# Kernel tuning notes

Measured on AMD Instinct MI355X. Metric: run time of the kernel, lower is better.

The kernel has to match this reference:

```python
import jax, jax.numpy as jnp
import numpy as np

B, L, IN_DIM, H, LAYERS = 16, 2048, 64, 512, 4
KERNELS = (5, 11, 23)
EPS_BN, EPS_LN = 1e-5, 1e-5


def setup_inputs() -> dict:
    key = jax.random.key(0)
    ks = jax.random.split(key, 16)
    def n(k, shape, s=0.02):
        return jax.random.normal(k, shape, jnp.float32) * s
    inp = {"x": jax.random.normal(ks[0], (B, L, IN_DIM), jnp.float32)}
    inp["Wp"] = n(ks[1], (H, IN_DIM), 0.1)
    inp["bp"] = jnp.zeros((H,), jnp.float32)
    inp["ln_g"] = jnp.ones((LAYERS, H), jnp.float32)
    inp["ln_b"] = jnp.zeros((LAYERS, H), jnp.float32)
    for i, k in enumerate(KERNELS):
        inp[f"conv_w{i}"] = n(ks[2 + i], (LAYERS, H, k), 0.1)  # depthwise kernels
        inp[f"conv_b{i}"] = jnp.zeros((LAYERS, H), jnp.float32)
    inp["bn_g"] = jnp.ones((LAYERS, 3, H), jnp.float32)
    inp["bn_b"] = jnp.zeros((LAYERS, 3, H), jnp.float32)
    inp["gate_W"] = n(ks[5], (LAYERS, 3, 3 * H), 0.02)
    inp["gate_b"] = jnp.zeros((LAYERS, 3), jnp.float32)
    inp["Wih"] = n(ks[6], (LAYERS, 3 * H, H), 0.04)  # GRU input weights (r,z,n)
    inp["Whh"] = n(ks[7], (LAYERS, 3 * H, H), 0.04)  # GRU hidden weights
    inp["bih"] = jnp.zeros((LAYERS, 3 * H), jnp.float32)
    inp["bhh"] = jnp.zeros((LAYERS, 3 * H), jnp.float32)
    return inp


def _layernorm(h, g, b):
    mu = h.mean(-1, keepdims=True)
    var = ((h - mu) ** 2).mean(-1, keepdims=True)
    return (h - mu) / jnp.sqrt(var + EPS_LN) * g + b


def _dwconv(h_bhl, w, b):
    # h_bhl: [B,H,L]; w: [H,k] depthwise; 'same' padding for odd k (pad=k//2)
    k = w.shape[-1]
    out = jax.lax.conv_general_dilated(
        h_bhl, w[:, None, :], (1,), [(k // 2, k // 2)],
        dimension_numbers=("NCH", "OIH", "NCH"), feature_group_count=h_bhl.shape[1])
    return out + b[None, :, None]


def _longconv_mix(h, conv_ws, conv_bs, bn_g, bn_b, gate_W, gate_b):
    # h: [B,L,H]
    ht = jnp.swapaxes(h, 1, 2)  # [B,H,L]
    bn_scale = 1.0 / jnp.sqrt(1.0 + EPS_BN)  # eval BN: running mean 0, var 1
    outs = []
    for i in range(len(conv_ws)):
        o = _dwconv(ht, conv_ws[i], conv_bs[i])
        o = o * (bn_g[i] * bn_scale)[None, :, None] + bn_b[i][None, :, None]
        outs.append(jax.nn.gelu(o, approximate=False))
    cat_t = jnp.swapaxes(jnp.concatenate(outs, axis=1), 1, 2)  # [B,L,3H]
    logits = cat_t @ gate_W.T + gate_b                          # [B,L,3]
    wgt = jax.nn.softmax(logits, axis=-1)
    stack = jnp.stack(outs, axis=1)                             # [B,3,H,L]
    out = jnp.einsum("bkhl,blk->bhl", stack, wgt)
    return jnp.swapaxes(out, 1, 2)  # [B,L,H]


def _gru(h, Wih, Whh, bih, bhh):
    # torch nn.GRU math, gate order r,z,n; h: [B,L,H]
    Bb, Ll, Hh = h.shape
    xg = jnp.swapaxes(h @ Wih.T + bih, 0, 1)  # [L,B,3H]
    def step(hp, x_t):
        hg = hp @ Whh.T + bhh
        xr, xz, xn = jnp.split(x_t, 3, axis=-1)
        hr, hz, hn = jnp.split(hg, 3, axis=-1)
        r = jax.nn.sigmoid(xr + hr)
        z = jax.nn.sigmoid(xz + hz)
        n = jnp.tanh(xn + r * hn)
        hnew = (1.0 - z) * n + z * hp
        return hnew, hnew
    _, ys = jax.lax.scan(step, jnp.zeros((Bb, Hh), h.dtype), xg)
    return jnp.swapaxes(ys, 0, 1)  # [B,L,H]


def reference(x, Wp, bp, ln_g, ln_b, conv_w0, conv_b0, conv_w1, conv_b1,
              conv_w2, conv_b2, bn_g, bn_b, gate_W, gate_b, Wih, Whh, bih, bhh):
    h = x @ Wp.T + bp  # input_proj: [B,L,H]
    for l in range(LAYERS):
        h = _layernorm(h, ln_g[l], ln_b[l])
        h = _longconv_mix(h,
                          (conv_w0[l], conv_w1[l], conv_w2[l]),
                          (conv_b0[l], conv_b1[l], conv_b2[l]),
                          bn_g[l], bn_b[l], gate_W[l], gate_b[l])
        out = _gru(h, Wih[l], Whh[l], bih[l], bhh[l])
        h = h + out  # residual (dropout=0 in eval)
    return h
```

## Files before the change

### kernel.cpp

```cpp
#include <hip/hip_runtime.h>
#include <hip/hip_bf16.h>


#define B_   16
#define L_   2048
#define IN_  64
#define H_   512
#define H3_  1536
#define NL_  4

typedef unsigned short u16;
typedef unsigned long long u64;
typedef short bf16x8 __attribute__((ext_vector_type(8)));
typedef float f32x4 __attribute__((ext_vector_type(4)));

__device__ __forceinline__ u16 f2bf(float f) {
  unsigned u = __float_as_uint(f);
  u = u + 0x7fffu + ((u >> 16) & 1u);
  return (u16)(u >> 16);
}
__device__ __forceinline__ float bf2f(u16 v) {
  return __uint_as_float(((unsigned)v) << 16);
}
__device__ __forceinline__ float gelu_exact(float x) {
  return 0.5f * x * (1.f + erff(x * 0.70710678118654752440f));
}
__device__ __forceinline__ float fast_sig(float x) {
  float e = __expf(-x);
  return __builtin_amdgcn_rcpf(1.f + e);
}
__device__ __forceinline__ float fast_tanh(float x) {
  x = fminf(fmaxf(x, -15.f), 15.f);
  float e = __expf(2.f * x);
  return (e - 1.f) * __builtin_amdgcn_rcpf(e + 1.f);
}
__device__ __forceinline__ float dotw(uint4 wp, float4 ha, float4 hc) {
  float acc;
  acc  = __uint_as_float(wp.x << 16)          * ha.x;
  acc += __uint_as_float(wp.x & 0xffff0000u)  * ha.y;
  acc += __uint_as_float(wp.y << 16)          * ha.z;
  acc += __uint_as_float(wp.y & 0xffff0000u)  * ha.w;
  acc += __uint_as_float(wp.z << 16)          * hc.x;
  acc += __uint_as_float(wp.z & 0xffff0000u)  * hc.y;
  acc += __uint_as_float(wp.w << 16)          * hc.z;
  acc += __uint_as_float(wp.w & 0xffff0000u)  * hc.w;
  return acc;
}

__global__ void k_init(u64* hst, int n) {
  int i = blockIdx.x * blockDim.x + threadIdx.x;
  if (i < n) hst[i] = 0ull;
}

__global__ void k_cvt(const float* __restrict__ in, u16* __restrict__ out, int n) {
  int i = blockIdx.x * blockDim.x + threadIdx.x;
  int stride = gridDim.x * blockDim.x;
  for (; i < n; i += stride) out[i] = f2bf(in[i]);
}

__global__ __launch_bounds__(512)
void k_proj(const float* __restrict__ x, const float* __restrict__ Wp,
            const float* __restrict__ bp, float* __restrict__ hb) {
  __shared__ float4 xs[128];
  const int tid = threadIdx.x;
  const size_t m0 = (size_t)blockIdx.x * 8;
  if (tid < 128) xs[tid] = ((const float4*)(x + m0 * IN_))[tid];
  __syncthreads();
  float4 wv[16];
  const float4* wp4 = (const float4*)(Wp + (size_t)tid * IN_);
#pragma unroll
  for (int i = 0; i < 16; ++i) wv[i] = wp4[i];
  float acc[8] = {0.f,0.f,0.f,0.f,0.f,0.f,0.f,0.f};
#pragma unroll
  for (int k = 0; k < 16; ++k) {
    float4 w4 = wv[k];
#pragma unroll
    for (int rr = 0; rr < 8; ++rr) {
      float4 xv = xs[rr * 16 + k];
      acc[rr] += w4.x * xv.x + w4.y * xv.y + w4.z * xv.z + w4.w * xv.w;
    }
  }
  float bpv = bp[tid];
#pragma unroll
  for (int rr = 0; rr < 8; ++rr) hb[(m0 + rr) * H_ + tid] = acc[rr] + bpv;
}

__global__ __launch_bounds__(256)
void k_ln(const float* __restrict__ hin, const float* __restrict__ g,
          const float* __restrict__ bta, float* __restrict__ lnout) {
  const int w = threadIdx.x >> 6, lane = threadIdx.x & 63;
  const size_t m = (size_t)blockIdx.x * 4 + w;
  const float4* src = (const float4*)(hin + m * H_);
  float4 a = src[lane * 2], c = src[lane * 2 + 1];
  float sm = a.x + a.y + a.z + a.w + c.x + c.y + c.z + c.w;
  float sq = a.x*a.x + a.y*a.y + a.z*a.z + a.w*a.w + c.x*c.x + c.y*c.y + c.z*c.z + c.w*c.w;
  sm += __shfl_xor(sm, 1);  sq += __shfl_xor(sq, 1);
  sm += __shfl_xor(sm, 2);  sq += __shfl_xor(sq, 2);
  sm += __shfl_xor(sm, 4);  sq += __shfl_xor(sq, 4);
  sm += __shfl_xor(sm, 8);  sq += __shfl_xor(sq, 8);
  sm += __shfl_xor(sm, 16); sq += __shfl_xor(sq, 16);
  sm += __shfl_xor(sm, 32); sq += __shfl_xor(sq, 32);
  float mu = sm * (1.f / 512.f);
  float var = sq * (1.f / 512.f) - mu * mu;
  float inv = 1.f / sqrtf(var + 1e-5f);
  const float4* g4 = (const float4*)g;
  const float4* b4 = (const float4*)bta;
  float4 ga = g4[lane * 2], gc = g4[lane * 2 + 1];
  float4 ba = b4[lane * 2], bc = b4[lane * 2 + 1];
  float4 oa, oc;
  oa.x = (a.x - mu) * inv * ga.x + ba.x;
  oa.y = (a.y - mu) * inv * ga.y + ba.y;
  oa.z = (a.z - mu) * inv * ga.z + ba.z;
  oa.w = (a.w - mu) * inv * ga.w + ba.w;
  oc.x = (c.x - mu) * inv * gc.x + bc.x;
  oc.y = (c.y - mu) * inv * gc.y + bc.y;
  oc.z = (c.z - mu) * inv * gc.z + bc.z;
  oc.w = (c.w - mu) * inv * gc.w + bc.w;
  float4* dst = (float4*)(lnout + m * H_);
  dst[lane * 2] = oa;
  dst[lane * 2 + 1] = oc;
}

__global__ __launch_bounds__(512)
void k_mix(const float* __restrict__ ln,
           const float* __restrict__ w0, const float* __restrict__ cb0,
           const float* __restrict__ w1, const float* __restrict__ cb1,
           const float* __restrict__ w2, const float* __restrict__ cb2,
           const float* __restrict__ bng, const float* __restrict__ bnb,
           const float* __restrict__ gW, const float* __restrict__ gb,
           u16* __restrict__ mixbf) {
  const int h = threadIdx.x;
  const int bi = blockIdx.x >> 11;
  const int t = blockIdx.x & (L_ - 1);
  const size_t mrow = (size_t)blockIdx.x;
  float v[23];
#pragma unroll
  for (int d = 0; d < 23; ++d) {
    int tt = t + d - 11;
    v[d] = (tt >= 0 && tt < L_) ? ln[((size_t)bi * L_ + tt) * H_ + h] : 0.f;
  }
  float o0 = cb0[h], o1 = cb1[h], o2 = cb2[h];
#pragma unroll
  for (int d = 0; d < 5; ++d) o0 += v[9 + d] * w0[h * 5 + d];
#pragma unroll
  for (int d = 0; d < 11; ++d) o1 += v[6 + d] * w1[h * 11 + d];
#pragma unroll
  for (int d = 0; d < 23; ++d) o2 += v[d] * w2[h * 23 + d];
  const float bscale = 0.99999500003749968f;
  o0 = o0 * (bng[0 * H_ + h] * bscale) + bnb[0 * H_ + h];
  o1 = o1 * (bng[1 * H_ + h] * bscale) + bnb[1 * H_ + h];
  o2 = o2 * (bng[2 * H_ + h] * bscale) + bnb[2 * H_ + h];
  o0 = gelu_exact(o0); o1 = gelu_exact(o1); o2 = gelu_exact(o2);
  float l0 = o0 * gW[0 * H3_ + h] + o1 * gW[0 * H3_ + H_ + h] + o2 * gW[0 * H3_ + 2 * H_ + h];
  float l1 = o0 * gW[1 * H3_ + h] + o1 * gW[1 * H3_ + H_ + h] + o2 * gW[1 * H3_ + 2 * H_ + h];
  float l2 = o0 * gW[2 * H3_ + h] + o1 * gW[2 * H3_ + H_ + h] + o2 * gW[2 * H3_ + 2 * H_ + h];
  l0 += __shfl_xor(l0, 1);  l1 += __shfl_xor(l1, 1);  l2 += __shfl_xor(l2, 1);
  l0 += __shfl_xor(l0, 2);  l1 += __shfl_xor(l1, 2);  l2 += __shfl_xor(l2, 2);
  l0 += __shfl_xor(l0, 4);  l1 += __shfl_xor(l1, 4);  l2 += __shfl_xor(l2, 4);
  l0 += __shfl_xor(l0, 8);  l1 += __shfl_xor(l1, 8);  l2 += __shfl_xor(l2, 8);
  l0 += __shfl_xor(l0, 16); l1 += __shfl_xor(l1, 16); l2 += __shfl_xor(l2, 16);
  l0 += __shfl_xor(l0, 32); l1 += __shfl_xor(l1, 32); l2 += __shfl_xor(l2, 32);
  __shared__ float red[8][3];
  const int w = h >> 6, lane = h & 63;
  if (lane == 0) { red[w][0] = l0; red[w][1] = l1; red[w][2] = l2; }
  __syncthreads();
  l0 = gb[0]; l1 = gb[1]; l2 = gb[2];
#pragma unroll
  for (int i = 0; i < 8; ++i) { l0 += red[i][0]; l1 += red[i][1]; l2 += red[i][2]; }
  float mx = fmaxf(l0, fmaxf(l1, l2));
  float e0 = expf(l0 - mx), e1 = expf(l1 - mx), e2 = expf(l2 - mx);
  float inv = 1.f / (e0 + e1 + e2);
  float out = (o0 * e0 + o1 * e1 + o2 * e2) * inv;
  mixbf[mrow * H_ + h] = f2bf(out);
}

__global__ __launch_bounds__(256)
void k_gemm(const u16* __restrict__ A, const u16* __restrict__ Bm,
            const float* __restrict__ bias, u16* __restrict__ C) {
  __shared__ u16 As[128 * 32];
  __shared__ u16 Bs[128 * 32];
  const int tid = threadIdx.x;
  const int bm = blockIdx.x / 12, bn = blockIdx.x % 12;
  const int m0 = bm * 128, n0 = bn * 128;
  const int w = tid >> 6, lane = tid & 63;
  const int wr = w >> 1, wc = w & 1;
  const int q = lane >> 4, r = lane & 15;
  f32x4 acc[4][4] = {};
  const uint4* Ag = (const uint4*)(A + (size_t)m0 * H_);
  const uint4* Bg = (const uint4*)(Bm + (size_t)n0 * H_);
  uint4* As4 = (uint4*)As;
  uint4* Bs4 = (uint4*)Bs;
  for (int ko = 0; ko < 16; ++ko) {
    __syncthreads();
#pragma unroll
    for (int i = 0; i < 2; ++i) {
      int j = tid + 256 * i;
      As4[j] = Ag[(size_t)(j >> 2) * 64 + (j & 3) + ko * 4];
      Bs4[j] = Bg[(size_t)(j >> 2) * 64 + (j & 3) + ko * 4];
    }
    __syncthreads();
    bf16x8 av[4], bv[4];
#pragma unroll
    for (int m = 0; m < 4; ++m) av[m] = *(const bf16x8*)&As[(wr * 64 + m * 16 + r) * 32 + q * 8];
#pragma unroll
    for (int n = 0; n < 4; ++n) bv[n] = *(const bf16x8*)&Bs[(wc * 64 + n * 16 + r) * 32 + q * 8];
#pragma unroll
    for (int m = 0; m < 4; ++m)
#pragma unroll
      for (int n = 0; n < 4; ++n)
        acc[m][n] = __builtin_amdgcn_mfma_f32_16x16x32_bf16(av[m], bv[n], acc[m][n], 0, 0, 0);
  }
#pragma unroll
  for (int n = 0; n < 4; ++n) {
    int col = n0 + wc * 64 + n * 16 + r;
    float bv_ = bias[col];
#pragma unroll
    for (int m = 0; m < 4; ++m) {
      int row = m0 + wr * 64 + m * 16 + q * 4;
#pragma unroll
      for (int i = 0; i < 4; ++i) {
        float v = acc[m][n][i] + bv_;
        C[(size_t)(row + i) * H3_ + col] = f2bf(v);
      }
    }
  }
}

__global__ __launch_bounds__(512, 1)
void k_gru(const float* __restrict__ Whh_l, const float* __restrict__ bhh_l,
           const u16* __restrict__ xg, const u16* __restrict__ mixbf,
           float* __restrict__ out_h, u64* hst, int tbase) {
  const int tid = threadIdx.x;
  const int wg = blockIdx.x;
  const int b = wg >> 4, s = wg & 15;
  const int w = tid >> 6, lane = tid & 63;
  const int g16 = lane >> 4, l16 = lane & 15;
  const int jj = 4 * w + g16;
  const int d_own = s * 32 + jj;
  const bool gl = (l16 == 0);

  __shared__ __align__(16) u16 w_lds[512][104];
  __shared__ __align__(16) float h_lds[2][576];

  {
    const float* s0 = Whh_l + ((size_t)0 * H_ + d_own) * H_ + l16 * 32;
    const float* s1 = Whh_l + ((size_t)1 * H_ + d_own) * H_ + l16 * 32;
    const float* s2 = Whh_l + ((size_t)2 * H_ + d_own) * H_ + l16 * 32;
#pragma unroll
    for (int c = 0; c < 4; ++c) {
      float4 a, v; u16* dst;
      a = *(const float4*)(s0 + c * 8); v = *(const float4*)(s0 + c * 8 + 4);
      dst = &w_lds[tid][c * 24 + 0];
      dst[0]=f2bf(a.x); dst[1]=f2bf(a.y); dst[2]=f2bf(a.z); dst[3]=f2bf(a.w);
      dst[4]=f2bf(v.x); dst[5]=f2bf(v.y); dst[6]=f2bf(v.z); dst[7]=f2bf(v.w);
      a = *(const float4*)(s1 + c * 8); v = *(const float4*)(s1 + c * 8 + 4);
      dst = &w_lds[tid][c * 24 + 8];
      dst[0]=f2bf(a.x); dst[1]=f2bf(a.y); dst[2]=f2bf(a.z); dst[3]=f2bf(a.w);
      dst[4]=f2bf(v.x); dst[5]=f2bf(v.y); dst[6]=f2bf(v.z); dst[7]=f2bf(v.w);
      a = *(const float4*)(s2 + c * 8); v = *(const float4*)(s2 + c * 8 + 4);
      dst = &w_lds[tid][c * 24 + 16];
      dst[0]=f2bf(a.x); dst[1]=f2bf(a.y); dst[2]=f2bf(a.z); dst[3]=f2bf(a.w);
      dst[4]=f2bf(v.x); dst[5]=f2bf(v.y); dst[6]=f2bf(v.z); dst[7]=f2bf(v.w);
    }
  }
  const float br_ = bhh_l[0 * H_ + d_own];
  const float bz_ = bhh_l[1 * H_ + d_own];
  const float bn_ = bhh_l[2 * H_ + d_own];

  h_lds[0][(tid >> 5) * 36 + (tid & 31)] = 0.f;
  float hp = 0.f;
  __syncthreads();

  const u16* xgp = xg + (size_t)b * L_ * H3_ + d_own;
  const u16* mxp = mixbf + (size_t)b * L_ * H_ + d_own;
  float* outp = out_h + (size_t)b * L_ * H_ + d_own;
  const char* wbase = (const char*)&w_lds[tid][0];

  uint4 wv[4][3];
#pragma unroll
  for (int c = 0; c < 4; ++c) {
    const int cp = (c + g16) & 3;
    wv[c][0] = *(const uint4*)(wbase + cp * 48);
    wv[c][1] = *(const uint4*)(wbase + cp * 48 + 16);
    wv[c][2] = *(const uint4*)(wbase + cp * 48 + 32);
  }
  u16 xr_c = 0, xz_c = 0, xn_c = 0, mx_c = 0;
  if (gl) {
    xr_c = xgp[0]; xz_c = xgp[H_]; xn_c = xgp[2 * H_]; mx_c = mxp[0];
  }

  for (int t = 0; t < L_; ++t) {
    const int cur = t & 1, nxt = cur ^ 1;
    const unsigned T = (unsigned)(tbase + t + 1);

    u16 xr_n = 0, xz_n = 0, xn_n = 0, mx_n = 0;
    if (gl && t + 1 < L_) {
      const u16* xq = xgp + (size_t)(t + 1) * H3_;
      xr_n = xq[0]; xz_n = xq[H_]; xn_n = xq[2 * H_];
      mx_n = mxp[(size_t)(t + 1) * H_];
    }

    const float* hb = &h_lds[cur][l16 * 36];
    float q0 = 0.f, q1 = 0.f, q2 = 0.f;
#pragma unroll
    for (int c = 0; c < 4; ++c) {
      const int cp = (c + g16) & 3;
      float4 ha = *(const float4*)(hb + cp * 8);
      float4 hc = *(const float4*)(hb + cp * 8 + 4);
      q0 += dotw(wv[c][0], ha, hc);
      q1 += dotw(wv[c][1], ha, hc);
      q2 += dotw(wv[c][2], ha, hc);
    }

#pragma unroll
    for (int c = 0; c < 4; ++c) {
      const int cp = (c + g16) & 3;
      wv[c][0] = *(const uint4*)(wbase + cp * 48);
      wv[c][1] = *(const uint4*)(wbase + cp * 48 + 16);
      wv[c][2] = *(const uint4*)(wbase + cp * 48 + 32);
    }

    q0 += __shfl_xor(q0, 1); q1 += __shfl_xor(q1, 1); q2 += __shfl_xor(q2, 1);
    q0 += __shfl_xor(q0, 2); q1 += __shfl_xor(q1, 2); q2 += __shfl_xor(q2, 2);
    q0 += __shfl_xor(q0, 4); q1 += __shfl_xor(q1, 4); q2 += __shfl_xor(q2, 4);
    q0 += __shfl_xor(q0, 8); q1 += __shfl_xor(q1, 8); q2 += __shfl_xor(q2, 8);

    if (gl) {
      float r = fast_sig(bf2f(xr_c) + q0 + br_);
      float z = fast_sig(bf2f(xz_c) + q1 + bz_);
      float n = fast_tanh(bf2f(xn_c) + r * (q2 + bn_));
      float hnew = n + z * (hp - n);
      hp = hnew;
      if (t + 1 < L_) {
        __hip_atomic_store(&hst[(size_t)nxt * 8192 + (b << 9) + d_own],
                           ((u64)T << 32) | (u64)__float_as_uint(hnew),
                           __ATOMIC_RELAXED, __HIP_MEMORY_SCOPE_AGENT);
        h_lds[nxt][s * 36 + jj] = hnew;
      }
      outp[(size_t)t * H_] = bf2f(mx_c) + hnew;
    }

    if (t + 1 < L_ && (tid >> 5) != s) {
      u64* sl = &hst[(size_t)nxt * 8192 + (b << 9) + tid];
      u64 v;
      do {
        v = __hip_atomic_load(sl, __ATOMIC_RELAXED, __HIP_MEMORY_SCOPE_AGENT);
      } while ((unsigned)(v >> 32) != T);
      h_lds[nxt][(tid >> 5) * 36 + (tid & 31)] = __uint_as_float((unsigned)v);
    }
    __syncthreads();

    xr_c = xr_n; xz_c = xz_n; xn_c = xn_n; mx_c = mx_n;
  }
}

extern "C" void kernel_launch(void* const* d_in, const int* in_sizes, int n_in,
                              void* d_out, int out_size, void* d_ws, size_t ws_size,
                              hipStream_t stream) {
  (void)in_sizes; (void)n_in; (void)out_size; (void)ws_size;
  const float* x    = (const float*)d_in[0];
  const float* Wp   = (const float*)d_in[1];
  const float* bp   = (const float*)d_in[2];
  const float* ln_g = (const float*)d_in[3];
  const float* ln_b = (const float*)d_in[4];
  const float* cw0  = (const float*)d_in[5];
  const float* cb0  = (const float*)d_in[6];
  const float* cw1  = (const float*)d_in[7];
  const float* cb1  = (const float*)d_in[8];
  const float* cw2  = (const float*)d_in[9];
  const float* cb2  = (const float*)d_in[10];
  const float* bng  = (const float*)d_in[11];
  const float* bnb  = (const float*)d_in[12];
  const float* gW   = (const float*)d_in[13];
  const float* gb   = (const float*)d_in[14];
  const float* Wih  = (const float*)d_in[15];
  const float* Whh  = (const float*)d_in[16];
  const float* bih  = (const float*)d_in[17];
  const float* bhh  = (const float*)d_in[18];

  char* ws = (char*)d_ws;
  u16*   xg    = (u16*)(ws + 0);
  float* ln    = (float*)(ws + 0);
  u16*   mixbf = (u16*)(ws + (size_t)96 * 1024 * 1024);
  u16*   wihbf = (u16*)(ws + (size_t)128 * 1024 * 1024);
  u64*   hst   = (u64*)(ws + (size_t)134 * 1024 * 1024);
  float* hbuf  = (float*)d_out;

  k_init<<<dim3(64), dim3(256), 0, stream>>>(hst, 2 * B_ * H_);
  k_cvt<<<dim3(3072), dim3(256), 0, stream>>>(Wih, wihbf, NL_ * H3_ * H_);
  k_proj<<<dim3(B_ * L_ / 8), dim3(512), 0, stream>>>(x, Wp, bp, hbuf);

  for (int l = 0; l < NL_; ++l) {
    k_ln<<<dim3(B_ * L_ / 4), dim3(256), 0, stream>>>(hbuf, ln_g + l * H_, ln_b + l * H_, ln);
    k_mix<<<dim3(B_ * L_), dim3(512), 0, stream>>>(ln,
        cw0 + l * H_ * 5,  cb0 + l * H_,
        cw1 + l * H_ * 11, cb1 + l * H_,
        cw2 + l * H_ * 23, cb2 + l * H_,
        bng + l * 3 * H_, bnb + l * 3 * H_,
        gW + l * 3 * H3_, gb + l * 3, mixbf);
    k_gemm<<<dim3((B_ * L_ / 128) * (H3_ / 128)), dim3(256), 0, stream>>>(
        mixbf, wihbf + (size_t)l * H3_ * H_, bih + l * H3_, xg);

    const float* whh_l = Whh + (size_t)l * H3_ * H_;
    const float* bhh_l = bhh + l * H3_;
    const u16* xg_c = xg;
    const u16* mix_c = mixbf;
    float* outp = hbuf;
    int tbase = l * L_;
    void* args[] = { (void*)&whh_l, (void*)&bhh_l, (void*)&xg_c, (void*)&mix_c,
                     (void*)&outp, (void*)&hst, (void*)&tbase };
    hipLaunchCooperativeKernel((void*)k_gru, dim3(B_ * 16), dim3(512), args, 0, stream);
  }
}
```

Before: 18.95 ms.

## Pack GRU hidden-state exchange as bf16 pairs with fewer polling lanes

After: 46.75 ms. 147% more time.

```diff
diff --git a/kernel.cpp b/kernel.cpp
--- a/kernel.cpp
+++ b/kernel.cpp
@@ -239,7 +239,7 @@
   const int d_own = s * 32 + jj;
   const bool gl = (l16 == 0);
 
-  __shared__ __align__(16) u16 w_lds[512][104];
+  __shared__ __align__(16) u16 w_lds[512][106];
   __shared__ __align__(16) float h_lds[2][576];
 
   {
@@ -331,22 +331,51 @@
       float n = fast_tanh(bf2f(xn_c) + r * (q2 + bn_));
       float hnew = n + z * (hp - n);
       hp = hnew;
+      unsigned myraw = (unsigned)f2bf(hnew);
+      unsigned peer  = (unsigned)__shfl((int)myraw, (lane + 16) & 63);
       if (t + 1 < L_) {
-        __hip_atomic_store(&hst[(size_t)nxt * 8192 + (b << 9) + d_own],
-                           ((u64)T << 32) | (u64)__float_as_uint(hnew),
-                           __ATOMIC_RELAXED, __HIP_MEMORY_SCOPE_AGENT);
+        if ((g16 & 1) == 0) {
+          int ell  = d_own >> 4;
+          int slot = (d_own & 15) >> 1;
+          u64 pv = ((u64)T << 32) | (u64)(myraw | (peer << 16));
+          __hip_atomic_store(&hst[(size_t)nxt * 4096 + (size_t)(ell * 16 + b) * 8 + slot],
+                             pv, __ATOMIC_RELAXED, __HIP_MEMORY_SCOPE_AGENT);
+        }
         h_lds[nxt][s * 36 + jj] = hnew;
       }
       outp[(size_t)t * H_] = bf2f(mx_c) + hnew;
     }
 
-    if (t + 1 < L_ && (tid >> 5) != s) {
-      u64* sl = &hst[(size_t)nxt * 8192 + (b << 9) + tid];
-      u64 v;
-      do {
-        v = __hip_atomic_load(sl, __ATOMIC_RELAXED, __HIP_MEMORY_SCOPE_AGENT);
-      } while ((unsigned)(v >> 32) != T);
-      h_lds[nxt][(tid >> 5) * 36 + (tid & 31)] = __uint_as_float((unsigned)v);
+    if (t + 1 < L_ && l16 == 1) {
+      const int ell = tid >> 4;
+      if ((ell >> 1) != s) {
+        u64* lp = &hst[(size_t)nxt * 4096 + (size_t)(ell * 16 + b) * 8];
+        u64 v0, v1, v2, v3, v4, v5, v6, v7;
+        bool ok;
+        do {
+          v0 = __hip_atomic_load(lp + 0, __ATOMIC_RELAXED, __HIP_MEMORY_SCOPE_AGENT);
+          v1 = __hip_atomic_load(lp + 1, __ATOMIC_RELAXED, __HIP_MEMORY_SCOPE_AGENT);
+          v2 = __hip_atomic_load(lp + 2, __ATOMIC_RELAXED, __HIP_MEMORY_SCOPE_AGENT);
+          v3 = __hip_atomic_load(lp + 3, __ATOMIC_RELAXED, __HIP_MEMORY_SCOPE_AGENT);
+          v4 = __hip_atomic_load(lp + 4, __ATOMIC_RELAXED, __HIP_MEMORY_SCOPE_AGENT);
+          v5 = __hip_atomic_load(lp + 5, __ATOMIC_RELAXED, __HIP_MEMORY_SCOPE_AGENT);
+          v6 = __hip_atomic_load(lp + 6, __ATOMIC_RELAXED, __HIP_MEMORY_SCOPE_AGENT);
+          v7 = __hip_atomic_load(lp + 7, __ATOMIC_RELAXED, __HIP_MEMORY_SCOPE_AGENT);
+          ok = ((unsigned)(v0 >> 32) == T) & ((unsigned)(v1 >> 32) == T)
+             & ((unsigned)(v2 >> 32) == T) & ((unsigned)(v3 >> 32) == T)
+             & ((unsigned)(v4 >> 32) == T) & ((unsigned)(v5 >> 32) == T)
+             & ((unsigned)(v6 >> 32) == T) & ((unsigned)(v7 >> 32) == T);
+        } while (!ok);
+        float* hd = &h_lds[nxt][(ell >> 1) * 36 + (ell & 1) * 16];
+        hd[0]  = bf2f((u16)v0); hd[1]  = bf2f((u16)(v0 >> 16));
+        hd[2]  = bf2f((u16)v1); hd[3]  = bf2f((u16)(v1 >> 16));
+        hd[4]  = bf2f((u16)v2); hd[5]  = bf2f((u16)(v2 >> 16));
+        hd[6]  = bf2f((u16)v3); hd[7]  = bf2f((u16)(v3 >> 16));
+        hd[8]  = bf2f((u16)v4); hd[9]  = bf2f((u16)(v4 >> 16));
+        hd[10] = bf2f((u16)v5); hd[11] = bf2f((u16)(v5 >> 16));
+        hd[12] = bf2f((u16)v6); hd[13] = bf2f((u16)(v6 >> 16));
+        hd[14] = bf2f((u16)v7); hd[15] = bf2f((u16)(v7 >> 16));
+      }
     }
     __syncthreads();
 
@@ -386,7 +415,7 @@
   u64*   hst   = (u64*)(ws + (size_t)134 * 1024 * 1024);
   float* hbuf  = (float*)d_out;
 
-  k_init<<<dim3(64), dim3(256), 0, stream>>>(hst, 2 * B_ * H_);
+  k_init<<<dim3(32), dim3(256), 0, stream>>>(hst, 8192);
   k_cvt<<<dim3(3072), dim3(256), 0, stream>>>(Wih, wihbf, NL_ * H3_ * H_);
   k_proj<<<dim3(B_ * L_ / 8), dim3(512), 0, stream>>>(x, Wp, bp, hbuf);
 
```

## Have each GRU lane poll global h-state directly and drop the per-step barrier

Applied to the files above, without the earlier changes.

New measurement: 71.69 ms. 278% more time.

```diff
diff --git a/kernel.cpp b/kernel.cpp
--- a/kernel.cpp
+++ b/kernel.cpp
@@ -13,6 +13,7 @@
 typedef unsigned long long u64;
 typedef short bf16x8 __attribute__((ext_vector_type(8)));
 typedef float f32x4 __attribute__((ext_vector_type(4)));
+typedef unsigned u32x4 __attribute__((ext_vector_type(4)));
 
 __device__ __forceinline__ u16 f2bf(float f) {
   unsigned u = __float_as_uint(f);
@@ -33,18 +34,6 @@
   x = fminf(fmaxf(x, -15.f), 15.f);
   float e = __expf(2.f * x);
   return (e - 1.f) * __builtin_amdgcn_rcpf(e + 1.f);
-}
-__device__ __forceinline__ float dotw(uint4 wp, float4 ha, float4 hc) {
-  float acc;
-  acc  = __uint_as_float(wp.x << 16)          * ha.x;
-  acc += __uint_as_float(wp.x & 0xffff0000u)  * ha.y;
-  acc += __uint_as_float(wp.y << 16)          * ha.z;
-  acc += __uint_as_float(wp.y & 0xffff0000u)  * ha.w;
-  acc += __uint_as_float(wp.z << 16)          * hc.x;
-  acc += __uint_as_float(wp.z & 0xffff0000u)  * hc.y;
-  acc += __uint_as_float(wp.w << 16)          * hc.z;
-  acc += __uint_as_float(wp.w & 0xffff0000u)  * hc.w;
-  return acc;
 }
 
 __global__ void k_init(u64* hst, int n) {
@@ -239,59 +228,44 @@
   const int d_own = s * 32 + jj;
   const bool gl = (l16 == 0);
 
-  __shared__ __align__(16) u16 w_lds[512][104];
-  __shared__ __align__(16) float h_lds[2][576];
+  __shared__ u32x4 w_lds[12][512];
 
   {
-    const float* s0 = Whh_l + ((size_t)0 * H_ + d_own) * H_ + l16 * 32;
-    const float* s1 = Whh_l + ((size_t)1 * H_ + d_own) * H_ + l16 * 32;
-    const float* s2 = Whh_l + ((size_t)2 * H_ + d_own) * H_ + l16 * 32;
-#pragma unroll
-    for (int c = 0; c < 4; ++c) {
-      float4 a, v; u16* dst;
-      a = *(const float4*)(s0 + c * 8); v = *(const float4*)(s0 + c * 8 + 4);
-      dst = &w_lds[tid][c * 24 + 0];
-      dst[0]=f2bf(a.x); dst[1]=f2bf(a.y); dst[2]=f2bf(a.z); dst[3]=f2bf(a.w);
-      dst[4]=f2bf(v.x); dst[5]=f2bf(v.y); dst[6]=f2bf(v.z); dst[7]=f2bf(v.w);
-      a = *(const float4*)(s1 + c * 8); v = *(const float4*)(s1 + c * 8 + 4);
-      dst = &w_lds[tid][c * 24 + 8];
-      dst[0]=f2bf(a.x); dst[1]=f2bf(a.y); dst[2]=f2bf(a.z); dst[3]=f2bf(a.w);
-      dst[4]=f2bf(v.x); dst[5]=f2bf(v.y); dst[6]=f2bf(v.z); dst[7]=f2bf(v.w);
-      a = *(const float4*)(s2 + c * 8); v = *(const float4*)(s2 + c * 8 + 4);
-      dst = &w_lds[tid][c * 24 + 16];
-      dst[0]=f2bf(a.x); dst[1]=f2bf(a.y); dst[2]=f2bf(a.z); dst[3]=f2bf(a.w);
-      dst[4]=f2bf(v.x); dst[5]=f2bf(v.y); dst[6]=f2bf(v.z); dst[7]=f2bf(v.w);
+    unsigned wu[48];
+#pragma unroll
+    for (int r3 = 0; r3 < 3; ++r3) {
+      const float4* src = (const float4*)(Whh_l + ((size_t)(r3 * H_ + d_own)) * H_ + l16 * 32);
+#pragma unroll
+      for (int c = 0; c < 8; ++c) {
+        float4 f = src[c];
+        wu[r3 * 16 + c * 2 + 0] = (unsigned)f2bf(f.x) | ((unsigned)f2bf(f.y) << 16);
+        wu[r3 * 16 + c * 2 + 1] = (unsigned)f2bf(f.z) | ((unsigned)f2bf(f.w) << 16);
+      }
+    }
+#pragma unroll
+    for (int c = 0; c < 12; ++c) {
+      u32x4 q = { wu[c * 4], wu[c * 4 + 1], wu[c * 4 + 2], wu[c * 4 + 3] };
+      w_lds[c][tid] = q;
     }
   }
   const float br_ = bhh_l[0 * H_ + d_own];
   const float bz_ = bhh_l[1 * H_ + d_own];
   const float bn_ = bhh_l[2 * H_ + d_own];
-
-  h_lds[0][(tid >> 5) * 36 + (tid & 31)] = 0.f;
-  float hp = 0.f;
   __syncthreads();
 
   const u16* xgp = xg + (size_t)b * L_ * H3_ + d_own;
   const u16* mxp = mixbf + (size_t)b * L_ * H_ + d_own;
   float* outp = out_h + (size_t)b * L_ * H_ + d_own;
-  const char* wbase = (const char*)&w_lds[tid][0];
-
-  uint4 wv[4][3];
-#pragma unroll
-  for (int c = 0; c < 4; ++c) {
-    const int cp = (c + g16) & 3;
-    wv[c][0] = *(const uint4*)(wbase + cp * 48);
-    wv[c][1] = *(const uint4*)(wbase + cp * 48 + 16);
-    wv[c][2] = *(const uint4*)(wbase + cp * 48 + 32);
-  }
+
+  float hp = 0.f;
   u16 xr_c = 0, xz_c = 0, xn_c = 0, mx_c = 0;
   if (gl) {
     xr_c = xgp[0]; xz_c = xgp[H_]; xn_c = xgp[2 * H_]; mx_c = mxp[0];
   }
 
   for (int t = 0; t < L_; ++t) {
-    const int cur = t & 1, nxt = cur ^ 1;
-    const unsigned T = (unsigned)(tbase + t + 1);
+    const unsigned Tc = (unsigned)(tbase + t);
+    const unsigned Tp = Tc + 1;
 
     u16 xr_n = 0, xz_n = 0, xn_n = 0, mx_n = 0;
     if (gl && t + 1 < L_) {
@@ -300,24 +274,38 @@
       mx_n = mxp[(size_t)(t + 1) * H_];
     }
 
-    const float* hb = &h_lds[cur][l16 * 36];
     float q0 = 0.f, q1 = 0.f, q2 = 0.f;
-#pragma unroll
-    for (int c = 0; c < 4; ++c) {
-      const int cp = (c + g16) & 3;
-      float4 ha = *(const float4*)(hb + cp * 8);
-      float4 hc = *(const float4*)(hb + cp * 8 + 4);
-      q0 += dotw(wv[c][0], ha, hc);
-      q1 += dotw(wv[c][1], ha, hc);
-      q2 += dotw(wv[c][2], ha, hc);
-    }
-
-#pragma unroll
-    for (int c = 0; c < 4; ++c) {
-      const int cp = (c + g16) & 3;
-      wv[c][0] = *(const uint4*)(wbase + cp * 48);
-      wv[c][1] = *(const uint4*)(wbase + cp * 48 + 16);
-      wv[c][2] = *(const uint4*)(wbase + cp * 48 + 32);
+    if (t > 0) {
+      u32x4 wq[12];
+#pragma unroll
+      for (int c = 0; c < 12; ++c) wq[c] = w_lds[c][tid];
+
+      const u64* sp = hst + (size_t)(Tc & 1) * 4096 + (size_t)b * 256 + l16 * 16;
+      u64 v[16];
+      unsigned mask = 0;
+      do {
+#pragma unroll
+        for (int j = 0; j < 16; ++j)
+          if (!(mask & (1u << j)))
+            v[j] = __hip_atomic_load(sp + j, __ATOMIC_RELAXED, __HIP_MEMORY_SCOPE_AGENT);
+#pragma unroll
+        for (int j = 0; j < 16; ++j)
+          if (!(mask & (1u << j)) && (unsigned)(v[j] >> 32) == Tc)
+            mask |= 1u << j;
+      } while (mask != 0xFFFFu);
+
+#pragma unroll
+      for (int j = 0; j < 16; ++j) {
+        const unsigned lo = (unsigned)v[j];
+        const float alo = __uint_as_float(lo << 16);
+        const float ahi = __uint_as_float(lo & 0xffff0000u);
+        const unsigned w0 = wq[j >> 2][j & 3];
+        const unsigned w1 = wq[(16 + j) >> 2][(16 + j) & 3];
+        const unsigned w2 = wq[(32 + j) >> 2][(32 + j) & 3];
+        q0 += __uint_as_float(w0 << 16) * alo + __uint_as_float(w0 & 0xffff0000u) * ahi;
+        q1 += __uint_as_float(w1 << 16) * alo + __uint_as_float(w1 & 0xffff0000u) * ahi;
+        q2 += __uint_as_float(w2 << 16) * alo + __uint_as_float(w2 & 0xffff0000u) * ahi;
+      }
     }
 
     q0 += __shfl_xor(q0, 1); q1 += __shfl_xor(q1, 1); q2 += __shfl_xor(q2, 1);
@@ -331,24 +319,15 @@
       float n = fast_tanh(bf2f(xn_c) + r * (q2 + bn_));
       float hnew = n + z * (hp - n);
       hp = hnew;
-      if (t + 1 < L_) {
-        __hip_atomic_store(&hst[(size_t)nxt * 8192 + (b << 9) + d_own],
-                           ((u64)T << 32) | (u64)__float_as_uint(hnew),
-                           __ATOMIC_RELAXED, __HIP_MEMORY_SCOPE_AGENT);
-        h_lds[nxt][s * 36 + jj] = hnew;
+      unsigned myraw = (unsigned)f2bf(hnew);
+      unsigned peer  = (unsigned)__shfl((int)myraw, (lane + 16) & 63);
+      if ((g16 & 1) == 0) {
+        u64 pv = ((u64)Tp << 32) | (u64)(myraw | (peer << 16));
+        __hip_atomic_store(hst + (size_t)(Tp & 1) * 4096 + (size_t)b * 256 + (d_own >> 1),
+                           pv, __ATOMIC_RELAXED, __HIP_MEMORY_SCOPE_AGENT);
       }
       outp[(size_t)t * H_] = bf2f(mx_c) + hnew;
     }
-
-    if (t + 1 < L_ && (tid >> 5) != s) {
-      u64* sl = &hst[(size_t)nxt * 8192 + (b << 9) + tid];
-      u64 v;
-      do {
-        v = __hip_atomic_load(sl, __ATOMIC_RELAXED, __HIP_MEMORY_SCOPE_AGENT);
-      } while ((unsigned)(v >> 32) != T);
-      h_lds[nxt][(tid >> 5) * 36 + (tid & 31)] = __uint_as_float((unsigned)v);
-    }
-    __syncthreads();
 
     xr_c = xr_n; xz_c = xz_n; xn_c = xn_n; mx_c = mx_n;
   }
@@ -386,7 +365,7 @@
   u64*   hst   = (u64*)(ws + (size_t)134 * 1024 * 1024);
   float* hbuf  = (float*)d_out;
 
-  k_init<<<dim3(64), dim3(256), 0, stream>>>(hst, 2 * B_ * H_);
+  k_init<<<dim3(32), dim3(256), 0, stream>>>(hst, 8192);
   k_cvt<<<dim3(3072), dim3(256), 0, stream>>>(Wih, wihbf, NL_ * H3_ * H_);
   k_proj<<<dim3(B_ * L_ / 8), dim3(512), 0, stream>>>(x, Wp, bp, hbuf);
 
```
